# Optimization experiments

Hardware: AMD Instinct MI355X
Metric: run time of the kernel (lower is better)

Reference implementation:

```python
import jax, jax.numpy as jnp
import numpy as np
from jax.ops import segment_sum

N_V = 50000   # vertices
N_E = 10000   # hyperedges
N_P = 800000  # incidence pairs
D_IN = 256
D_OUT = 256
NEG_SLOPE = 0.01


def setup_inputs() -> dict:
    key = jax.random.key(0)
    k1, k2, k3, k4, k5 = jax.random.split(key, 5)
    X = jax.random.normal(k1, (N_V, D_IN), dtype=jnp.float32)
    W = jax.random.normal(k2, (D_IN, D_OUT), dtype=jnp.float32) * (1.0 / np.sqrt(D_IN))
    b = jax.random.normal(k3, (D_OUT,), dtype=jnp.float32) * 0.01
    v_idx = jax.random.randint(k4, (N_P,), 0, N_V, dtype=jnp.int32)
    e_idx = jax.random.randint(k5, (N_P,), 0, N_E, dtype=jnp.int32)
    return {"X": X, "W": W, "b": b, "v_idx": v_idx, "e_idx": e_idx,
            "num_hyperedges": N_E}


def _mean_scatter(msg, idx, num_segments):
    # segment mean with count clamped to >=1 (empty segments -> 0)
    s = segment_sum(msg, idx, num_segments=num_segments)
    cnt = segment_sum(jnp.ones((msg.shape[0],), msg.dtype), idx,
                      num_segments=num_segments)
    return s / jnp.maximum(cnt, 1.0)[:, None]


def reference(X, W, b, v_idx, e_idx, num_hyperedges):
    # theta: linear projection  [N_V, D_OUT]
    H = X @ W + b
    # v2e mean: hyperedge features from member vertices
    e_feat = _mean_scatter(H[v_idx], e_idx, num_hyperedges)   # [N_E, D_OUT]
    # e2v mean: vertex features from incident hyperedges
    v_feat = _mean_scatter(e_feat[e_idx], v_idx, X.shape[0])  # [N_V, D_OUT]
    # leaky relu, default negative slope 0.01
    return jnp.where(v_feat >= 0, v_feat, NEG_SLOPE * v_feat)
```

## Files before the change

### kernel.cpp

```cpp
#include <hip/hip_runtime.h>

#define D 256
#define NEG_SLOPE 0.01f
#define E_PAD 192
#define V_PAD 64
#define EB 32
#define VB 64
#define NBE 313
#define NBV 782
#define CAP_E 3328
#define CAP_V 1536
#define CHUNK 8192

__device__ __forceinline__ unsigned short f2bf(float f) {
    union { float f; unsigned u; } x; x.f = f;
    unsigned r = x.u + 0x7fffu + ((x.u >> 16) & 1u);
    return (unsigned short)(r >> 16);
}
__device__ __forceinline__ float bf2f(unsigned short h) {
    union { float f; unsigned u; } x; x.u = ((unsigned)h) << 16;
    return x.f;
}

__global__ __launch_bounds__(256) void cvt_kernel(
        const float* __restrict__ X, unsigned short* __restrict__ Xh, int n4) {
    int i = blockIdx.x * blockDim.x + threadIdx.x;
    if (i < n4) {
        float4 v = ((const float4*)X)[i];
        ushort4 h;
        h.x = f2bf(v.x); h.y = f2bf(v.y); h.z = f2bf(v.z); h.w = f2bf(v.w);
        ((ushort4*)Xh)[i] = h;
    }
}

__global__ __launch_bounds__(256) void part_kernel(
        const int* __restrict__ v_idx, const int* __restrict__ e_idx,
        int* __restrict__ bc_e, int* __restrict__ bc_v,
        unsigned* __restrict__ pe, unsigned* __restrict__ pv, int n_p) {
    __shared__ int he[NBE], hv[NBV], beb[NBE], bvb[NBV];
    const int tid = threadIdx.x;
    const int base = blockIdx.x * CHUNK;
    for (int i = tid; i < NBE; i += 256) he[i] = 0;
    for (int i = tid; i < NBV; i += 256) hv[i] = 0;
    __syncthreads();
    #pragma unroll 4
    for (int r = 0; r < CHUNK / 256; ++r) {
        int p = base + r * 256 + tid;
        if (p < n_p) {
            atomicAdd(&he[e_idx[p] >> 5], 1);
            atomicAdd(&hv[v_idx[p] >> 6], 1);
        }
    }
    __syncthreads();
    for (int b = tid; b < NBE; b += 256) {
        int c = he[b];
        beb[b] = c ? atomicAdd(&bc_e[b], c) : 0;
        he[b] = 0;
    }
    for (int b = tid; b < NBV; b += 256) {
        int c = hv[b];
        bvb[b] = c ? atomicAdd(&bc_v[b], c) : 0;
        hv[b] = 0;
    }
    __syncthreads();
    #pragma unroll 4
    for (int r = 0; r < CHUNK / 256; ++r) {
        int p = base + r * 256 + tid;
        if (p < n_p) {
            int e = e_idx[p], v = v_idx[p];
            int b1 = e >> 5;
            int s1 = beb[b1] + atomicAdd(&he[b1], 1);
            if (s1 < CAP_E) pe[(size_t)b1 * CAP_E + s1] = (unsigned)v | ((unsigned)e << 16);
            int b2 = v >> 6;
            int s2 = bvb[b2] + atomicAdd(&hv[b2], 1);
            if (s2 < CAP_V) pv[(size_t)b2 * CAP_V + s2] = (unsigned)e | ((unsigned)v << 16);
        }
    }
}

__global__ __launch_bounds__(256) void build_e_kernel(
        const unsigned* __restrict__ pe, const int* __restrict__ bc_e,
        unsigned short* __restrict__ e_adj, int* __restrict__ e_fill, int n_e) {
    __shared__ unsigned short adj[EB * E_PAD];
    __shared__ int cnt[EB];
    const int b = blockIdx.x;
    const int tid = threadIdx.x;
    const int e0 = b * EB;
    int m = n_e - e0; if (m > EB) m = EB;
    for (int i = tid; i < EB; i += 256) cnt[i] = 0;
    __syncthreads();
    int total = bc_e[b]; if (total > CAP_E) total = CAP_E;
    for (int i = tid; i < total; i += 256) {
        unsigned p = pe[(size_t)b * CAP_E + i];
        int v = (int)(p & 0xFFFFu);
        int el = (int)(p >> 16) - e0;
        int s = atomicAdd(&cnt[el], 1);
        if (s < E_PAD) adj[el * E_PAD + s] = (unsigned short)v;
    }
    __syncthreads();
    unsigned* gout = (unsigned*)(e_adj + (size_t)e0 * E_PAD);
    const unsigned* lin = (const unsigned*)adj;
    int words = m * E_PAD / 2;
    for (int j = tid; j < words; j += 256) gout[j] = lin[j];
    for (int el = tid; el < m; el += 256) {
        int c = cnt[el]; if (c > E_PAD) c = E_PAD;
        e_fill[e0 + el] = c;
    }
}

__global__ __launch_bounds__(256) void build_v_kernel(
        const unsigned* __restrict__ pv, const int* __restrict__ bc_v,
        unsigned short* __restrict__ v_adj, int* __restrict__ v_fill, int n_v) {
    __shared__ unsigned short adj[VB * V_PAD];
    __shared__ int cnt[VB];
    const int b = blockIdx.x;
    const int tid = threadIdx.x;
    const int v0 = b * VB;
    int m = n_v - v0; if (m > VB) m = VB;
    for (int i = tid; i < VB; i += 256) cnt[i] = 0;
    __syncthreads();
    int total = bc_v[b]; if (total > CAP_V) total = CAP_V;
    for (int i = tid; i < total; i += 256) {
        unsigned p = pv[(size_t)b * CAP_V + i];
        int e = (int)(p & 0xFFFFu);
        int vl = (int)(p >> 16) - v0;
        int s = atomicAdd(&cnt[vl], 1);
        if (s < V_PAD) adj[vl * V_PAD + s] = (unsigned short)e;
    }
    __syncthreads();
    unsigned* gout = (unsigned*)(v_adj + (size_t)v0 * V_PAD);
    const unsigned* lin = (const unsigned*)adj;
    int words = m * V_PAD / 2;
    for (int j = tid; j < words; j += 256) gout[j] = lin[j];
    for (int vl = tid; vl < m; vl += 256) {
        int c = cnt[vl]; if (c > V_PAD) c = V_PAD;
        v_fill[v0 + vl] = c;
    }
}

__global__ __launch_bounds__(256) void v2e_kernel(
        const unsigned short* __restrict__ Xh, const int* __restrict__ e_fill,
        const unsigned short* __restrict__ e_adj, float* __restrict__ Xagg, int n_e) {
    int seg = blockIdx.x * 4 + (threadIdx.x >> 6);
    if (seg >= n_e) return;
    int lane = threadIdx.x & 63;
    int cnt = e_fill[seg];
    const unsigned short* adj = e_adj + (size_t)seg * E_PAD;
    float4 acc = make_float4(0.f, 0.f, 0.f, 0.f);
    int i = 0;
    for (; i + 8 <= cnt; i += 8) {
        int v0 = adj[i], v1 = adj[i+1], v2 = adj[i+2], v3 = adj[i+3];
        int v4 = adj[i+4], v5 = adj[i+5], v6 = adj[i+6], v7 = adj[i+7];
        ushort4 a0 = *(const ushort4*)(Xh + (size_t)v0 * D + lane * 4);
        ushort4 a1 = *(const ushort4*)(Xh + (size_t)v1 * D + lane * 4);
        ushort4 a2 = *(const ushort4*)(Xh + (size_t)v2 * D + lane * 4);
        ushort4 a3 = *(const ushort4*)(Xh + (size_t)v3 * D + lane * 4);
        ushort4 a4 = *(const ushort4*)(Xh + (size_t)v4 * D + lane * 4);
        ushort4 a5 = *(const ushort4*)(Xh + (size_t)v5 * D + lane * 4);
        ushort4 a6 = *(const ushort4*)(Xh + (size_t)v6 * D + lane * 4);
        ushort4 a7 = *(const ushort4*)(Xh + (size_t)v7 * D + lane * 4);
        acc.x += (bf2f(a0.x) + bf2f(a1.x)) + (bf2f(a2.x) + bf2f(a3.x))
               + (bf2f(a4.x) + bf2f(a5.x)) + (bf2f(a6.x) + bf2f(a7.x));
        acc.y += (bf2f(a0.y) + bf2f(a1.y)) + (bf2f(a2.y) + bf2f(a3.y))
               + (bf2f(a4.y) + bf2f(a5.y)) + (bf2f(a6.y) + bf2f(a7.y));
        acc.z += (bf2f(a0.z) + bf2f(a1.z)) + (bf2f(a2.z) + bf2f(a3.z))
               + (bf2f(a4.z) + bf2f(a5.z)) + (bf2f(a6.z) + bf2f(a7.z));
        acc.w += (bf2f(a0.w) + bf2f(a1.w)) + (bf2f(a2.w) + bf2f(a3.w))
               + (bf2f(a4.w) + bf2f(a5.w)) + (bf2f(a6.w) + bf2f(a7.w));
    }
    for (; i < cnt; ++i) {
        int v = adj[i];
        ushort4 a = *(const ushort4*)(Xh + (size_t)v * D + lane * 4);
        acc.x += bf2f(a.x); acc.y += bf2f(a.y); acc.z += bf2f(a.z); acc.w += bf2f(a.w);
    }
    int c = cnt < 1 ? 1 : cnt;
    float inv = 1.0f / (float)c;
    acc.x *= inv; acc.y *= inv; acc.z *= inv; acc.w *= inv;
    *(float4*)(Xagg + (size_t)seg * D + lane * 4) = acc;
}

#define BM 64
#define BN 64
#define BK 64
#define SAK 68
#define SBN 68

__global__ __launch_bounds__(256) void gemm_kernel(
        const float* __restrict__ A, const float* __restrict__ B,
        const float* __restrict__ bias, const int* __restrict__ e_cnt,
        unsigned short* __restrict__ C, int M) {
    __shared__ float As[BM * SAK];
    __shared__ float Bs[BK * SBN];
    const int tid = threadIdx.x;
    const int tx = tid & 15, ty = tid >> 4;
    const int m0 = blockIdx.y * BM;
    const int n0 = blockIdx.x * BN;

    float acc[4][4] = {};

    for (int k0 = 0; k0 < D; k0 += BK) {
        #pragma unroll
        for (int r = 0; r < 4; ++r) {
            int l  = (tid + r * 256) * 4;
            int am = l >> 6;
            int ak = l & 63;
            int grow = m0 + am;
            float4 v = make_float4(0.f, 0.f, 0.f, 0.f);
            if (grow < M) v = *(const float4*)(A + (size_t)grow * D + k0 + ak);
            *(float4*)(&As[am * SAK + ak]) = v;
        }
        #pragma unroll
        for (int r = 0; r < 4; ++r) {
            int l  = (tid + r * 256) * 4;
            int bk = l >> 6;
            int bn = l & 63;
            float4 v = *(const float4*)(B + (size_t)(k0 + bk) * D + n0 + bn);
            *(float4*)(&Bs[bk * SBN + bn]) = v;
        }
        __syncthreads();

        #pragma unroll 8
        for (int kk = 0; kk < BK; ++kk) {
            float a0 = As[(ty * 4 + 0) * SAK + kk];
            float a1 = As[(ty * 4 + 1) * SAK + kk];
            float a2 = As[(ty * 4 + 2) * SAK + kk];
            float a3 = As[(ty * 4 + 3) * SAK + kk];
            float4 bv = *(const float4*)(Bs + kk * SBN + tx * 4);
            acc[0][0] += a0 * bv.x; acc[0][1] += a0 * bv.y; acc[0][2] += a0 * bv.z; acc[0][3] += a0 * bv.w;
            acc[1][0] += a1 * bv.x; acc[1][1] += a1 * bv.y; acc[1][2] += a1 * bv.z; acc[1][3] += a1 * bv.w;
            acc[2][0] += a2 * bv.x; acc[2][1] += a2 * bv.y; acc[2][2] += a2 * bv.z; acc[2][3] += a2 * bv.w;
            acc[3][0] += a3 * bv.x; acc[3][1] += a3 * bv.y; acc[3][2] += a3 * bv.z; acc[3][3] += a3 * bv.w;
        }
        __syncthreads();
    }

    float4 bb = *(const float4*)(bias + n0 + tx * 4);
    #pragma unroll
    for (int i = 0; i < 4; ++i) {
        int row = m0 + ty * 4 + i;
        if (row < M) {
            bool nonempty = e_cnt[row] > 0;
            ushort4 o;
            o.x = f2bf(nonempty ? acc[i][0] + bb.x : 0.f);
            o.y = f2bf(nonempty ? acc[i][1] + bb.y : 0.f);
            o.z = f2bf(nonempty ? acc[i][2] + bb.z : 0.f);
            o.w = f2bf(nonempty ? acc[i][3] + bb.w : 0.f);
            *(ushort4*)(C + (size_t)row * D + n0 + tx * 4) = o;
        }
    }
}

__global__ __launch_bounds__(256) void e2v_kernel(
        const unsigned short* __restrict__ Eh, const int* __restrict__ v_fill,
        const unsigned short* __restrict__ v_adj, float* __restrict__ out, int n_v) {
    int seg = blockIdx.x * 4 + (threadIdx.x >> 6);
    if (seg >= n_v) return;
    int lane = threadIdx.x & 63;
    int cnt = v_fill[seg];
    const unsigned short* adj = v_adj + (size_t)seg * V_PAD;
    float4 acc = make_float4(0.f, 0.f, 0.f, 0.f);
    int i = 0;
    for (; i + 8 <= cnt; i += 8) {
        int e0 = adj[i], e1 = adj[i+1], e2 = adj[i+2], e3 = adj[i+3];
        int e4 = adj[i+4], e5 = adj[i+5], e6 = adj[i+6], e7 = adj[i+7];
        ushort4 a0 = *(const ushort4*)(Eh + (size_t)e0 * D + lane * 4);
        ushort4 a1 = *(const ushort4*)(Eh + (size_t)e1 * D + lane * 4);
        ushort4 a2 = *(const ushort4*)(Eh + (size_t)e2 * D + lane * 4);
        ushort4 a3 = *(const ushort4*)(Eh + (size_t)e3 * D + lane * 4);
        ushort4 a4 = *(const ushort4*)(Eh + (size_t)e4 * D + lane * 4);
        ushort4 a5 = *(const ushort4*)(Eh + (size_t)e5 * D + lane * 4);
        ushort4 a6 = *(const ushort4*)(Eh + (size_t)e6 * D + lane * 4);
        ushort4 a7 = *(const ushort4*)(Eh + (size_t)e7 * D + lane * 4);
        acc.x += (bf2f(a0.x) + bf2f(a1.x)) + (bf2f(a2.x) + bf2f(a3.x))
               + (bf2f(a4.x) + bf2f(a5.x)) + (bf2f(a6.x) + bf2f(a7.x));
        acc.y += (bf2f(a0.y) + bf2f(a1.y)) + (bf2f(a2.y) + bf2f(a3.y))
               + (bf2f(a4.y) + bf2f(a5.y)) + (bf2f(a6.y) + bf2f(a7.y));
        acc.z += (bf2f(a0.z) + bf2f(a1.z)) + (bf2f(a2.z) + bf2f(a3.z))
               + (bf2f(a4.z) + bf2f(a5.z)) + (bf2f(a6.z) + bf2f(a7.z));
        acc.w += (bf2f(a0.w) + bf2f(a1.w)) + (bf2f(a2.w) + bf2f(a3.w))
               + (bf2f(a4.w) + bf2f(a5.w)) + (bf2f(a6.w) + bf2f(a7.w));
    }
    for (; i < cnt; ++i) {
        int e = adj[i];
        ushort4 a = *(const ushort4*)(Eh + (size_t)e * D + lane * 4);
        acc.x += bf2f(a.x); acc.y += bf2f(a.y); acc.z += bf2f(a.z); acc.w += bf2f(a.w);
    }
    int c = cnt < 1 ? 1 : cnt;
    float inv = 1.0f / (float)c;
    acc.x *= inv; acc.y *= inv; acc.z *= inv; acc.w *= inv;
    float4 o;
    o.x = acc.x >= 0.f ? acc.x : NEG_SLOPE * acc.x;
    o.y = acc.y >= 0.f ? acc.y : NEG_SLOPE * acc.y;
    o.z = acc.z >= 0.f ? acc.z : NEG_SLOPE * acc.z;
    o.w = acc.w >= 0.f ? acc.w : NEG_SLOPE * acc.w;
    *(float4*)(out + (size_t)seg * D + lane * 4) = o;
}

extern "C" void kernel_launch(void* const* d_in, const int* in_sizes, int n_in,
                              void* d_out, int out_size, void* d_ws, size_t ws_size,
                              hipStream_t stream) {
    const float* X    = (const float*)d_in[0];
    const float* W    = (const float*)d_in[1];
    const float* bias = (const float*)d_in[2];
    const int* v_idx  = (const int*)d_in[3];
    const int* e_idx  = (const int*)d_in[4];
    const int n_v = in_sizes[0] / D;
    const int n_p = in_sizes[3];
    const int n_e = 10000;

    char* w = (char*)d_ws;
    size_t off = 0;
    auto alloc = [&](size_t bytes) -> void* {
        void* p = w + off;
        off = (off + bytes + 255) & ~(size_t)255;
        return p;
    };
    unsigned short* Xh  = (unsigned short*)alloc((size_t)n_v * D * sizeof(unsigned short));
    float* Xagg         = (float*)alloc((size_t)n_e * D * sizeof(float));
    unsigned short* Eh  = (unsigned short*)alloc((size_t)n_e * D * sizeof(unsigned short));
    unsigned short* e_adj = (unsigned short*)alloc((size_t)n_e * E_PAD * sizeof(unsigned short));
    unsigned short* v_adj = (unsigned short*)alloc((size_t)n_v * V_PAD * sizeof(unsigned short));
    unsigned* pe   = (unsigned*)alloc((size_t)NBE * CAP_E * sizeof(unsigned));
    unsigned* pv   = (unsigned*)alloc((size_t)NBV * CAP_V * sizeof(unsigned));
    int*   fills   = (int*)alloc((size_t)(n_e + n_v) * sizeof(int));
    int*   e_fill  = fills;
    int*   v_fill  = e_fill + n_e;
    int*   bc      = (int*)alloc((size_t)(NBE + NBV) * sizeof(int));
    int*   bc_e    = bc;
    int*   bc_v    = bc + NBE;

    hipMemsetAsync(bc, 0, (size_t)(NBE + NBV) * sizeof(int), stream);

    int n4 = n_v * D / 4;
    cvt_kernel<<<(n4 + 255) / 256, 256, 0, stream>>>(X, Xh, n4);

    part_kernel<<<(n_p + CHUNK - 1) / CHUNK, 256, 0, stream>>>(
        v_idx, e_idx, bc_e, bc_v, pe, pv, n_p);
    build_e_kernel<<<NBE, 256, 0, stream>>>(pe, bc_e, e_adj, e_fill, n_e);
    build_v_kernel<<<NBV, 256, 0, stream>>>(pv, bc_v, v_adj, v_fill, n_v);

    v2e_kernel<<<(n_e + 3) / 4, 256, 0, stream>>>(Xh, e_fill, e_adj, Xagg, n_e);

    dim3 ggrid(D / BN, (n_e + BM - 1) / BM);
    gemm_kernel<<<ggrid, 256, 0, stream>>>(Xagg, W, bias, e_fill, Eh, n_e);

    e2v_kernel<<<(n_v + 3) / 4, 256, 0, stream>>>(Eh, v_fill, v_adj, (float*)d_out, n_v);
}
```

Baseline: 282.7 us.

## Slice bf16 vertex table by feature column and fuse vertex adjacency build into e2v

The bf16 copy of X is stored as 8 column slices of 32 features each. v2e runs one grid column per slice, with 16 lanes per hyperedge, so every slice of the gather table (about 3.2 MB) can stay resident in cache while it is read. The separate build_v kernel is removed: e2v now builds each block's vertex adjacency lists in shared memory from the partitioned pairs and gathers straight from them, which drops one launch and the v_adj global round trip. In exchange, the adjacency indices for each hyperedge are re-read once per slice, and each v2e load is narrower (ushort2 instead of ushort4).

```diff
diff --git a/kernel.cpp b/kernel.cpp
--- a/kernel.cpp
+++ b/kernel.cpp
@@ -11,6 +11,8 @@
 #define CAP_E 3328
 #define CAP_V 1536
 #define CHUNK 8192
+#define NS 8
+#define DS 32
 
 __device__ __forceinline__ unsigned short f2bf(float f) {
     union { float f; unsigned u; } x; x.f = f;
@@ -23,14 +25,16 @@
 }
 
 __global__ __launch_bounds__(256) void cvt_kernel(
-        const float* __restrict__ X, unsigned short* __restrict__ Xh, int n4) {
+        const float* __restrict__ X, unsigned short* __restrict__ Xhs, int n_v) {
     int i = blockIdx.x * blockDim.x + threadIdx.x;
-    if (i < n4) {
-        float4 v = ((const float4*)X)[i];
-        ushort4 h;
-        h.x = f2bf(v.x); h.y = f2bf(v.y); h.z = f2bf(v.z); h.w = f2bf(v.w);
-        ((ushort4*)Xh)[i] = h;
-    }
+    if (i >= n_v * 64) return;
+    int v = i >> 6;
+    int d4 = (i & 63) * 4;
+    float4 val = *(const float4*)(X + (size_t)v * D + d4);
+    ushort4 h;
+    h.x = f2bf(val.x); h.y = f2bf(val.y); h.z = f2bf(val.z); h.w = f2bf(val.w);
+    int s = d4 >> 5, wd = d4 & 31;
+    *(ushort4*)(Xhs + (size_t)s * n_v * DS + (size_t)v * DS + wd) = h;
 }
 
 __global__ __launch_bounds__(256) void part_kernel(
@@ -108,75 +112,45 @@
     }
 }
 
-__global__ __launch_bounds__(256) void build_v_kernel(
-        const unsigned* __restrict__ pv, const int* __restrict__ bc_v,
-        unsigned short* __restrict__ v_adj, int* __restrict__ v_fill, int n_v) {
-    __shared__ unsigned short adj[VB * V_PAD];
-    __shared__ int cnt[VB];
-    const int b = blockIdx.x;
-    const int tid = threadIdx.x;
-    const int v0 = b * VB;
-    int m = n_v - v0; if (m > VB) m = VB;
-    for (int i = tid; i < VB; i += 256) cnt[i] = 0;
-    __syncthreads();
-    int total = bc_v[b]; if (total > CAP_V) total = CAP_V;
-    for (int i = tid; i < total; i += 256) {
-        unsigned p = pv[(size_t)b * CAP_V + i];
-        int e = (int)(p & 0xFFFFu);
-        int vl = (int)(p >> 16) - v0;
-        int s = atomicAdd(&cnt[vl], 1);
-        if (s < V_PAD) adj[vl * V_PAD + s] = (unsigned short)e;
-    }
-    __syncthreads();
-    unsigned* gout = (unsigned*)(v_adj + (size_t)v0 * V_PAD);
-    const unsigned* lin = (const unsigned*)adj;
-    int words = m * V_PAD / 2;
-    for (int j = tid; j < words; j += 256) gout[j] = lin[j];
-    for (int vl = tid; vl < m; vl += 256) {
-        int c = cnt[vl]; if (c > V_PAD) c = V_PAD;
-        v_fill[v0 + vl] = c;
-    }
-}
-
 __global__ __launch_bounds__(256) void v2e_kernel(
-        const unsigned short* __restrict__ Xh, const int* __restrict__ e_fill,
-        const unsigned short* __restrict__ e_adj, float* __restrict__ Xagg, int n_e) {
-    int seg = blockIdx.x * 4 + (threadIdx.x >> 6);
-    if (seg >= n_e) return;
-    int lane = threadIdx.x & 63;
-    int cnt = e_fill[seg];
-    const unsigned short* adj = e_adj + (size_t)seg * E_PAD;
-    float4 acc = make_float4(0.f, 0.f, 0.f, 0.f);
+        const unsigned short* __restrict__ Xhs, const int* __restrict__ e_fill,
+        const unsigned short* __restrict__ e_adj, float* __restrict__ Xagg,
+        int n_e, int n_v) {
+    const int s   = blockIdx.x;
+    const int grp = threadIdx.x >> 4;
+    const int sub = threadIdx.x & 15;
+    const int e   = blockIdx.y * 16 + grp;
+    if (e >= n_e) return;
+    const unsigned short* tab = Xhs + (size_t)s * n_v * DS + (sub << 1);
+    const unsigned short* adj = e_adj + (size_t)e * E_PAD;
+    int cnt = e_fill[e];
+    float ax = 0.f, ay = 0.f;
     int i = 0;
     for (; i + 8 <= cnt; i += 8) {
-        int v0 = adj[i], v1 = adj[i+1], v2 = adj[i+2], v3 = adj[i+3];
+        int v0 = adj[i],   v1 = adj[i+1], v2 = adj[i+2], v3 = adj[i+3];
         int v4 = adj[i+4], v5 = adj[i+5], v6 = adj[i+6], v7 = adj[i+7];
-        ushort4 a0 = *(const ushort4*)(Xh + (size_t)v0 * D + lane * 4);
-        ushort4 a1 = *(const ushort4*)(Xh + (size_t)v1 * D + lane * 4);
-        ushort4 a2 = *(const ushort4*)(Xh + (size_t)v2 * D + lane * 4);
-        ushort4 a3 = *(const ushort4*)(Xh + (size_t)v3 * D + lane * 4);
-        ushort4 a4 = *(const ushort4*)(Xh + (size_t)v4 * D + lane * 4);
-        ushort4 a5 = *(const ushort4*)(Xh + (size_t)v5 * D + lane * 4);
-        ushort4 a6 = *(const ushort4*)(Xh + (size_t)v6 * D + lane * 4);
-        ushort4 a7 = *(const ushort4*)(Xh + (size_t)v7 * D + lane * 4);
-        acc.x += (bf2f(a0.x) + bf2f(a1.x)) + (bf2f(a2.x) + bf2f(a3.x))
-               + (bf2f(a4.x) + bf2f(a5.x)) + (bf2f(a6.x) + bf2f(a7.x));
-        acc.y += (bf2f(a0.y) + bf2f(a1.y)) + (bf2f(a2.y) + bf2f(a3.y))
-               + (bf2f(a4.y) + bf2f(a5.y)) + (bf2f(a6.y) + bf2f(a7.y));
-        acc.z += (bf2f(a0.z) + bf2f(a1.z)) + (bf2f(a2.z) + bf2f(a3.z))
-               + (bf2f(a4.z) + bf2f(a5.z)) + (bf2f(a6.z) + bf2f(a7.z));
-        acc.w += (bf2f(a0.w) + bf2f(a1.w)) + (bf2f(a2.w) + bf2f(a3.w))
-               + (bf2f(a4.w) + bf2f(a5.w)) + (bf2f(a6.w) + bf2f(a7.w));
+        ushort2 a0 = *(const ushort2*)(tab + (size_t)v0 * DS);
+        ushort2 a1 = *(const ushort2*)(tab + (size_t)v1 * DS);
+        ushort2 a2 = *(const ushort2*)(tab + (size_t)v2 * DS);
+        ushort2 a3 = *(const ushort2*)(tab + (size_t)v3 * DS);
+        ushort2 a4 = *(const ushort2*)(tab + (size_t)v4 * DS);
+        ushort2 a5 = *(const ushort2*)(tab + (size_t)v5 * DS);
+        ushort2 a6 = *(const ushort2*)(tab + (size_t)v6 * DS);
+        ushort2 a7 = *(const ushort2*)(tab + (size_t)v7 * DS);
+        ax += (bf2f(a0.x) + bf2f(a1.x)) + (bf2f(a2.x) + bf2f(a3.x))
+            + (bf2f(a4.x) + bf2f(a5.x)) + (bf2f(a6.x) + bf2f(a7.x));
+        ay += (bf2f(a0.y) + bf2f(a1.y)) + (bf2f(a2.y) + bf2f(a3.y))
+            + (bf2f(a4.y) + bf2f(a5.y)) + (bf2f(a6.y) + bf2f(a7.y));
     }
     for (; i < cnt; ++i) {
         int v = adj[i];
-        ushort4 a = *(const ushort4*)(Xh + (size_t)v * D + lane * 4);
-        acc.x += bf2f(a.x); acc.y += bf2f(a.y); acc.z += bf2f(a.z); acc.w += bf2f(a.w);
+        ushort2 a = *(const ushort2*)(tab + (size_t)v * DS);
+        ax += bf2f(a.x); ay += bf2f(a.y);
     }
     int c = cnt < 1 ? 1 : cnt;
     float inv = 1.0f / (float)c;
-    acc.x *= inv; acc.y *= inv; acc.z *= inv; acc.w *= inv;
-    *(float4*)(Xagg + (size_t)seg * D + lane * 4) = acc;
+    float2 o; o.x = ax * inv; o.y = ay * inv;
+    *(float2*)(Xagg + (size_t)e * D + s * DS + (sub << 1)) = o;
 }
 
 #define BM 64
@@ -251,49 +225,68 @@
 }
 
 __global__ __launch_bounds__(256) void e2v_kernel(
-        const unsigned short* __restrict__ Eh, const int* __restrict__ v_fill,
-        const unsigned short* __restrict__ v_adj, float* __restrict__ out, int n_v) {
-    int seg = blockIdx.x * 4 + (threadIdx.x >> 6);
-    if (seg >= n_v) return;
-    int lane = threadIdx.x & 63;
-    int cnt = v_fill[seg];
-    const unsigned short* adj = v_adj + (size_t)seg * V_PAD;
-    float4 acc = make_float4(0.f, 0.f, 0.f, 0.f);
-    int i = 0;
-    for (; i + 8 <= cnt; i += 8) {
-        int e0 = adj[i], e1 = adj[i+1], e2 = adj[i+2], e3 = adj[i+3];
-        int e4 = adj[i+4], e5 = adj[i+5], e6 = adj[i+6], e7 = adj[i+7];
-        ushort4 a0 = *(const ushort4*)(Eh + (size_t)e0 * D + lane * 4);
-        ushort4 a1 = *(const ushort4*)(Eh + (size_t)e1 * D + lane * 4);
-        ushort4 a2 = *(const ushort4*)(Eh + (size_t)e2 * D + lane * 4);
-        ushort4 a3 = *(const ushort4*)(Eh + (size_t)e3 * D + lane * 4);
-        ushort4 a4 = *(const ushort4*)(Eh + (size_t)e4 * D + lane * 4);
-        ushort4 a5 = *(const ushort4*)(Eh + (size_t)e5 * D + lane * 4);
-        ushort4 a6 = *(const ushort4*)(Eh + (size_t)e6 * D + lane * 4);
-        ushort4 a7 = *(const ushort4*)(Eh + (size_t)e7 * D + lane * 4);
-        acc.x += (bf2f(a0.x) + bf2f(a1.x)) + (bf2f(a2.x) + bf2f(a3.x))
-               + (bf2f(a4.x) + bf2f(a5.x)) + (bf2f(a6.x) + bf2f(a7.x));
-        acc.y += (bf2f(a0.y) + bf2f(a1.y)) + (bf2f(a2.y) + bf2f(a3.y))
-               + (bf2f(a4.y) + bf2f(a5.y)) + (bf2f(a6.y) + bf2f(a7.y));
-        acc.z += (bf2f(a0.z) + bf2f(a1.z)) + (bf2f(a2.z) + bf2f(a3.z))
-               + (bf2f(a4.z) + bf2f(a5.z)) + (bf2f(a6.z) + bf2f(a7.z));
-        acc.w += (bf2f(a0.w) + bf2f(a1.w)) + (bf2f(a2.w) + bf2f(a3.w))
-               + (bf2f(a4.w) + bf2f(a5.w)) + (bf2f(a6.w) + bf2f(a7.w));
-    }
-    for (; i < cnt; ++i) {
-        int e = adj[i];
-        ushort4 a = *(const ushort4*)(Eh + (size_t)e * D + lane * 4);
-        acc.x += bf2f(a.x); acc.y += bf2f(a.y); acc.z += bf2f(a.z); acc.w += bf2f(a.w);
-    }
-    int c = cnt < 1 ? 1 : cnt;
-    float inv = 1.0f / (float)c;
-    acc.x *= inv; acc.y *= inv; acc.z *= inv; acc.w *= inv;
-    float4 o;
-    o.x = acc.x >= 0.f ? acc.x : NEG_SLOPE * acc.x;
-    o.y = acc.y >= 0.f ? acc.y : NEG_SLOPE * acc.y;
-    o.z = acc.z >= 0.f ? acc.z : NEG_SLOPE * acc.z;
-    o.w = acc.w >= 0.f ? acc.w : NEG_SLOPE * acc.w;
-    *(float4*)(out + (size_t)seg * D + lane * 4) = o;
+        const unsigned short* __restrict__ Eh, const unsigned* __restrict__ pv,
+        const int* __restrict__ bc_v, float* __restrict__ out, int n_v) {
+    __shared__ unsigned short adj[VB * V_PAD];
+    __shared__ int cnt[VB];
+    const int b = blockIdx.x;
+    const int tid = threadIdx.x;
+    const int v0 = b * VB;
+    for (int i = tid; i < VB; i += 256) cnt[i] = 0;
+    __syncthreads();
+    int total = bc_v[b]; if (total > CAP_V) total = CAP_V;
+    for (int i = tid; i < total; i += 256) {
+        unsigned p = pv[(size_t)b * CAP_V + i];
+        int e = (int)(p & 0xFFFFu);
+        int vl = (int)(p >> 16) - v0;
+        int s = atomicAdd(&cnt[vl], 1);
+        if (s < V_PAD) adj[vl * V_PAD + s] = (unsigned short)e;
+    }
+    __syncthreads();
+    const int wave = tid >> 6, lane = tid & 63;
+    for (int r = 0; r < VB / 4; ++r) {
+        int vl = r * 4 + wave;
+        int v = v0 + vl;
+        if (v >= n_v) continue;
+        int c = cnt[vl]; if (c > V_PAD) c = V_PAD;
+        const unsigned short* a = adj + vl * V_PAD;
+        float4 acc = make_float4(0.f, 0.f, 0.f, 0.f);
+        int i = 0;
+        for (; i + 8 <= c; i += 8) {
+            int e0 = a[i],   e1 = a[i+1], e2 = a[i+2], e3 = a[i+3];
+            int e4 = a[i+4], e5 = a[i+5], e6 = a[i+6], e7 = a[i+7];
+            ushort4 a0 = *(const ushort4*)(Eh + (size_t)e0 * D + lane * 4);
+            ushort4 a1 = *(const ushort4*)(Eh + (size_t)e1 * D + lane * 4);
+            ushort4 a2 = *(const ushort4*)(Eh + (size_t)e2 * D + lane * 4);
+            ushort4 a3 = *(const ushort4*)(Eh + (size_t)e3 * D + lane * 4);
+            ushort4 a4 = *(const ushort4*)(Eh + (size_t)e4 * D + lane * 4);
+            ushort4 a5 = *(const ushort4*)(Eh + (size_t)e5 * D + lane * 4);
+            ushort4 a6 = *(const ushort4*)(Eh + (size_t)e6 * D + lane * 4);
+            ushort4 a7 = *(const ushort4*)(Eh + (size_t)e7 * D + lane * 4);
+            acc.x += (bf2f(a0.x) + bf2f(a1.x)) + (bf2f(a2.x) + bf2f(a3.x))
+                   + (bf2f(a4.x) + bf2f(a5.x)) + (bf2f(a6.x) + bf2f(a7.x));
+            acc.y += (bf2f(a0.y) + bf2f(a1.y)) + (bf2f(a2.y) + bf2f(a3.y))
+                   + (bf2f(a4.y) + bf2f(a5.y)) + (bf2f(a6.y) + bf2f(a7.y));
+            acc.z += (bf2f(a0.z) + bf2f(a1.z)) + (bf2f(a2.z) + bf2f(a3.z))
+                   + (bf2f(a4.z) + bf2f(a5.z)) + (bf2f(a6.z) + bf2f(a7.z));
+            acc.w += (bf2f(a0.w) + bf2f(a1.w)) + (bf2f(a2.w) + bf2f(a3.w))
+                   + (bf2f(a4.w) + bf2f(a5.w)) + (bf2f(a6.w) + bf2f(a7.w));
+        }
+        for (; i < c; ++i) {
+            int e = a[i];
+            ushort4 x = *(const ushort4*)(Eh + (size_t)e * D + lane * 4);
+            acc.x += bf2f(x.x); acc.y += bf2f(x.y); acc.z += bf2f(x.z); acc.w += bf2f(x.w);
+        }
+        int cc = c < 1 ? 1 : c;
+        float inv = 1.0f / (float)cc;
+        acc.x *= inv; acc.y *= inv; acc.z *= inv; acc.w *= inv;
+        float4 o;
+        o.x = acc.x >= 0.f ? acc.x : NEG_SLOPE * acc.x;
+        o.y = acc.y >= 0.f ? acc.y : NEG_SLOPE * acc.y;
+        o.z = acc.z >= 0.f ? acc.z : NEG_SLOPE * acc.z;
+        o.w = acc.w >= 0.f ? acc.w : NEG_SLOPE * acc.w;
+        *(float4*)(out + (size_t)v * D + lane * 4) = o;
+    }
 }
 
 extern "C" void kernel_launch(void* const* d_in, const int* in_sizes, int n_in,
@@ -315,34 +308,30 @@
         off = (off + bytes + 255) & ~(size_t)255;
         return p;
     };
-    unsigned short* Xh  = (unsigned short*)alloc((size_t)n_v * D * sizeof(unsigned short));
+    unsigned short* Xhs = (unsigned short*)alloc((size_t)NS * n_v * DS * sizeof(unsigned short));
     float* Xagg         = (float*)alloc((size_t)n_e * D * sizeof(float));
     unsigned short* Eh  = (unsigned short*)alloc((size_t)n_e * D * sizeof(unsigned short));
     unsigned short* e_adj = (unsigned short*)alloc((size_t)n_e * E_PAD * sizeof(unsigned short));
-    unsigned short* v_adj = (unsigned short*)alloc((size_t)n_v * V_PAD * sizeof(unsigned short));
     unsigned* pe   = (unsigned*)alloc((size_t)NBE * CAP_E * sizeof(unsigned));
     unsigned* pv   = (unsigned*)alloc((size_t)NBV * CAP_V * sizeof(unsigned));
-    int*   fills   = (int*)alloc((size_t)(n_e + n_v) * sizeof(int));
-    int*   e_fill  = fills;
-    int*   v_fill  = e_fill + n_e;
+    int*   e_fill  = (int*)alloc((size_t)n_e * sizeof(int));
     int*   bc      = (int*)alloc((size_t)(NBE + NBV) * sizeof(int));
     int*   bc_e    = bc;
     int*   bc_v    = bc + NBE;
 
     hipMemsetAsync(bc, 0, (size_t)(NBE + NBV) * sizeof(int), stream);
 
-    int n4 = n_v * D / 4;
-    cvt_kernel<<<(n4 + 255) / 256, 256, 0, stream>>>(X, Xh, n4);
+    cvt_kernel<<<(n_v * 64 + 255) / 256, 256, 0, stream>>>(X, Xhs, n_v);
 
     part_kernel<<<(n_p + CHUNK - 1) / CHUNK, 256, 0, stream>>>(
         v_idx, e_idx, bc_e, bc_v, pe, pv, n_p);
     build_e_kernel<<<NBE, 256, 0, stream>>>(pe, bc_e, e_adj, e_fill, n_e);
-    build_v_kernel<<<NBV, 256, 0, stream>>>(pv, bc_v, v_adj, v_fill, n_v);
-
-    v2e_kernel<<<(n_e + 3) / 4, 256, 0, stream>>>(Xh, e_fill, e_adj, Xagg, n_e);
+
+    dim3 vgrid(NS, (n_e + 15) / 16);
+    v2e_kernel<<<vgrid, 256, 0, stream>>>(Xhs, e_fill, e_adj, Xagg, n_e, n_v);
 
     dim3 ggrid(D / BN, (n_e + BM - 1) / BM);
     gemm_kernel<<<ggrid, 256, 0, stream>>>(Xagg, W, bias, e_fill, Eh, n_e);
 
-    e2v_kernel<<<(n_v + 3) / 4, 256, 0, stream>>>(Eh, v_fill, v_adj, (float*)d_out, n_v);
-}
+    e2v_kernel<<<NBV, 256, 0, stream>>>(Eh, pv, bc_v, (float*)d_out, n_v);
+}
```

New measurement: 281.7 us. No clear change (-0.3%).
